# Optimization experiments

Hardware: AMD Instinct MI355X
Metric: run time of the kernel (lower is better)

The kernel has to match this reference:

```python
import jax, jax.numpy as jnp
import numpy as np

N = 100000   # total nodes across the batch of glycan graphs
E = 300000   # directed edges
H = 256      # hidden_dim
D = 128      # embedding_dim (projection out)
L = 3        # num_layers
G = 10000    # number of graphs in the batch
V = 14       # monosaccharide vocab size
EPS = 1e-5   # BatchNorm eps


def setup_inputs() -> dict:
    key = jax.random.key(0)
    ks = jax.random.split(key, 12)
    s = 1.0 / np.sqrt(H)
    node_ids = jax.random.randint(ks[0], (N,), 0, V, dtype=jnp.int32)
    edge_index = jax.random.randint(ks[1], (2, E), 0, N, dtype=jnp.int32)
    batch_ids = jnp.sort(jax.random.randint(ks[2], (N,), 0, G, dtype=jnp.int32))
    return {
        "node_ids": node_ids,
        "edge_index": edge_index,
        "batch_ids": batch_ids,
        "emb": jax.random.normal(ks[3], (V, H), jnp.float32),
        "Ws": jax.random.normal(ks[4], (L, H, H), jnp.float32) * s,
        "bs": jax.random.normal(ks[5], (L, H), jnp.float32) * 0.01,
        "gammas": 1.0 + 0.1 * jax.random.normal(ks[6], (L, H), jnp.float32),
        "betas": 0.1 * jax.random.normal(ks[7], (L, H), jnp.float32),
        "run_mean": 0.1 * jax.random.normal(ks[8], (L, H), jnp.float32),
        "run_var": jax.random.uniform(ks[9], (L, H), jnp.float32) + 0.5,
        "projW": jax.random.normal(ks[10], (H, D), jnp.float32) * s,
        "projb": jax.random.normal(ks[11], (D,), jnp.float32) * 0.01,
    }


def reference(node_ids, edge_index, batch_ids, emb, Ws, bs, gammas, betas,
              run_mean, run_var, projW, projb):
    # --- GCN normalization with self-loops (PyG GCNConv defaults) ---
    src, dst = edge_index[0], edge_index[1]
    loops = jnp.arange(N, dtype=src.dtype)
    src_f = jnp.concatenate([src, loops])  # [E+N]
    dst_f = jnp.concatenate([dst, loops])
    deg = jax.ops.segment_sum(jnp.ones_like(dst_f, dtype=jnp.float32), dst_f,
                              num_segments=N)
    dinv = jnp.where(deg > 0, jax.lax.rsqrt(deg), 0.0)
    norm = dinv[src_f] * dinv[dst_f]       # [E+N]

    x = emb[node_ids]                       # [N, H]
    for l in range(L):
        h = x @ Ws[l]                       # GCNConv linear transform
        msg = h[src_f] * norm[:, None]      # [E+N, H] gathered messages
        h = jax.ops.segment_sum(msg, dst_f, num_segments=N) + bs[l]
        # BatchNorm1d (eval mode: running stats) + ReLU; dropout is identity in eval
        h = (h - run_mean[l]) * jax.lax.rsqrt(run_var[l] + EPS) * gammas[l] + betas[l]
        x = jax.nn.relu(h)

    # global_mean_pool over graph assignment
    counts = jax.ops.segment_sum(jnp.ones((N,), jnp.float32), batch_ids,
                                 num_segments=G)
    sums = jax.ops.segment_sum(x, batch_ids, num_segments=G)   # [G, H]
    pooled = sums / jnp.maximum(counts, 1.0)[:, None]
    return pooled @ projW + projb           # [G, D]
```

## Files before the change

kernel.cpp:

```cpp
#include <hip/hip_runtime.h>

#define HDIM 256
#define DDIM 128
#define VSZ 14

typedef __bf16 bf16x8 __attribute__((ext_vector_type(8)));
typedef float f32x4 __attribute__((ext_vector_type(4)));

static __device__ __forceinline__ unsigned short f2bf(float f) {
  unsigned u = __builtin_bit_cast(unsigned, f);
  u += 0x7FFF + ((u >> 16) & 1);
  return (unsigned short)(u >> 16);
}
static __device__ __forceinline__ unsigned pack2(float a, float b) {
  return (unsigned)f2bf(a) | ((unsigned)f2bf(b) << 16);
}
static __device__ __forceinline__ void ub8(uint4 p, float* o) {
  o[0] = __builtin_bit_cast(float, p.x << 16);
  o[1] = __builtin_bit_cast(float, p.x & 0xFFFF0000u);
  o[2] = __builtin_bit_cast(float, p.y << 16);
  o[3] = __builtin_bit_cast(float, p.y & 0xFFFF0000u);
  o[4] = __builtin_bit_cast(float, p.z << 16);
  o[5] = __builtin_bit_cast(float, p.z & 0xFFFF0000u);
  o[6] = __builtin_bit_cast(float, p.w << 16);
  o[7] = __builtin_bit_cast(float, p.w & 0xFFFF0000u);
}


__global__ void k_count(const int* __restrict__ dst, int* __restrict__ cnt, int E) {
  int i = blockIdx.x * 256 + threadIdx.x;
  if (i < E) atomicAdd(&cnt[dst[i]], 1);
}

__global__ void k_scan_chunk(const int* __restrict__ cnt, int* __restrict__ off,
                             int* __restrict__ bsum, float* __restrict__ dinv, int n) {
  __shared__ int s[256];
  int i = blockIdx.x * 256 + threadIdx.x;
  int v = (i < n) ? cnt[i] : 0;
  if (i < n) dinv[i] = rsqrtf((float)(v + 1));
  s[threadIdx.x] = v;
  __syncthreads();
  for (int d = 1; d < 256; d <<= 1) {
    int add = (threadIdx.x >= d) ? s[threadIdx.x - d] : 0;
    __syncthreads();
    s[threadIdx.x] += add;
    __syncthreads();
  }
  if (i < n) off[i] = s[threadIdx.x] - v;
  if (threadIdx.x == 255) bsum[blockIdx.x] = s[255];
}

__global__ void k_scan_bsum(int* bsum, int nb) {
  if (threadIdx.x == 0) {
    int acc = 0;
    for (int b = 0; b < nb; ++b) { int t = bsum[b]; bsum[b] = acc; acc += t; }
  }
}

__global__ void k_scan_add(int* __restrict__ off, const int* __restrict__ bsum,
                           int* __restrict__ cnt, int n, int E) {
  int i = blockIdx.x * 256 + threadIdx.x;
  if (i < n) {
    off[i] += bsum[i >> 8];
    cnt[i] = 0;
  } else if (i == n) {
    off[n] = E;
  }
}

__global__ void k_fill(const int* __restrict__ src, const int* __restrict__ dst,
                       const int* __restrict__ ids, const float* __restrict__ dinv,
                       const int* __restrict__ off, int* __restrict__ cur,
                       int4* __restrict__ edata, int E) {
  int i = blockIdx.x * 256 + threadIdx.x;
  if (i >= E) return;
  int d = dst[i];
  int p = off[d] + atomicAdd(&cur[d], 1);
  int s = src[i];
  int4 v;
  v.x = s;
  v.y = ids[s];
  v.z = __builtin_bit_cast(int, dinv[s]);
  v.w = 0;
  edata[p] = v;
}


__global__ void k_embw(const float* __restrict__ emb, const float* __restrict__ W0,
                       float* __restrict__ embW) {
  int t = blockIdx.x, j = threadIdx.x;
  float acc = 0.f;
  for (int k = 0; k < HDIM; ++k) acc = fmaf(emb[t * HDIM + k], W0[k * HDIM + j], acc);
  embW[t * HDIM + j] = acc;
}

__global__ void k_bnc(const float* __restrict__ bs, const float* __restrict__ g,
                      const float* __restrict__ be, const float* __restrict__ mu,
                      const float* __restrict__ va, float* __restrict__ A,
                      float* __restrict__ B) {
  int i = blockIdx.x * HDIM + threadIdx.x;
  float a = g[i] * rsqrtf(va[i] + 1e-5f);
  A[i] = a;
  B[i] = (bs[i] - mu[i]) * a + be[i];
}

__global__ __launch_bounds__(256) void k_wcvt(const float* __restrict__ W,
                                              unsigned short* __restrict__ Wt) {
  __shared__ float tile[32][33];
  int bx = blockIdx.x * 32, by = blockIdx.y * 32;
  int tx = threadIdx.x & 31, ty = threadIdx.x >> 5;
#pragma unroll
  for (int i = 0; i < 4; ++i)
    tile[ty + i * 8][tx] = W[(size_t)(by + ty + i * 8) * HDIM + bx + tx];
  __syncthreads();
#pragma unroll
  for (int i = 0; i < 4; ++i)
    Wt[(size_t)(bx + ty + i * 8) * HDIM + by + tx] = f2bf(tile[tx][ty + i * 8]);
}


__global__ __launch_bounds__(256) void k_layer1(
    const int* __restrict__ ids, const float* __restrict__ embW,
    const int* __restrict__ off, const int4* __restrict__ edata,
    const float* __restrict__ dinv,
    const float* __restrict__ A, const float* __restrict__ B,
    unsigned short* __restrict__ Y, int n) {
  __shared__ unsigned short lw[VSZ * HDIM];
  for (int i = threadIdx.x; i < VSZ * HDIM; i += 256) lw[i] = f2bf(embW[i]);
  __syncthreads();
  int j = (threadIdx.x & 31) * 8;
  float4 a0 = *reinterpret_cast<const float4*>(&A[j]);
  float4 a1 = *reinterpret_cast<const float4*>(&A[j + 4]);
  float4 b0 = *reinterpret_cast<const float4*>(&B[j]);
  float4 b1 = *reinterpret_cast<const float4*>(&B[j + 4]);
  int nb = (n + 7) >> 3;
  for (int b = blockIdx.x; b < nb; b += gridDim.x) {
    int v = b * 8 + (threadIdx.x >> 5);
    if (v >= n) continue;
    float dv = dinv[v];
    float s = dv * dv;
    float acc[8], m[8];
    uint4 x = *reinterpret_cast<const uint4*>(&lw[ids[v] * HDIM + j]);
    ub8(x, acc);
#pragma unroll
    for (int i = 0; i < 8; ++i) acc[i] *= s;
    int e = off[v], e1 = off[v + 1];
    for (; e + 3 < e1; e += 4) {
      int4 d0 = edata[e], d1 = edata[e + 1], d2 = edata[e + 2], d3 = edata[e + 3];
      uint4 g0 = *reinterpret_cast<const uint4*>(&lw[d0.y * HDIM + j]);
      uint4 g1 = *reinterpret_cast<const uint4*>(&lw[d1.y * HDIM + j]);
      uint4 g2 = *reinterpret_cast<const uint4*>(&lw[d2.y * HDIM + j]);
      uint4 g3 = *reinterpret_cast<const uint4*>(&lw[d3.y * HDIM + j]);
      float w0 = dv * __builtin_bit_cast(float, d0.z);
      float w1 = dv * __builtin_bit_cast(float, d1.z);
      float w2 = dv * __builtin_bit_cast(float, d2.z);
      float w3 = dv * __builtin_bit_cast(float, d3.z);
      ub8(g0, m);
#pragma unroll
      for (int i = 0; i < 8; ++i) acc[i] = fmaf(w0, m[i], acc[i]);
      ub8(g1, m);
#pragma unroll
      for (int i = 0; i < 8; ++i) acc[i] = fmaf(w1, m[i], acc[i]);
      ub8(g2, m);
#pragma unroll
      for (int i = 0; i < 8; ++i) acc[i] = fmaf(w2, m[i], acc[i]);
      ub8(g3, m);
#pragma unroll
      for (int i = 0; i < 8; ++i) acc[i] = fmaf(w3, m[i], acc[i]);
    }
    for (; e < e1; ++e) {
      int4 d0 = edata[e];
      uint4 g0 = *reinterpret_cast<const uint4*>(&lw[d0.y * HDIM + j]);
      float w0 = dv * __builtin_bit_cast(float, d0.z);
      ub8(g0, m);
#pragma unroll
      for (int i = 0; i < 8; ++i) acc[i] = fmaf(w0, m[i], acc[i]);
    }
    float o[8];
    o[0] = fmaxf(fmaf(acc[0], a0.x, b0.x), 0.f);
    o[1] = fmaxf(fmaf(acc[1], a0.y, b0.y), 0.f);
    o[2] = fmaxf(fmaf(acc[2], a0.z, b0.z), 0.f);
    o[3] = fmaxf(fmaf(acc[3], a0.w, b0.w), 0.f);
    o[4] = fmaxf(fmaf(acc[4], a1.x, b1.x), 0.f);
    o[5] = fmaxf(fmaf(acc[5], a1.y, b1.y), 0.f);
    o[6] = fmaxf(fmaf(acc[6], a1.z, b1.z), 0.f);
    o[7] = fmaxf(fmaf(acc[7], a1.w, b1.w), 0.f);
    uint4 st;
    st.x = pack2(o[0], o[1]);
    st.y = pack2(o[2], o[3]);
    st.z = pack2(o[4], o[5]);
    st.w = pack2(o[6], o[7]);
    *reinterpret_cast<uint4*>(&Y[(size_t)v * HDIM + j]) = st;
  }
}


__global__ __launch_bounds__(256) void k_agg(
    const unsigned short* __restrict__ X, const int* __restrict__ off,
    const int4* __restrict__ edata, const float* __restrict__ dinv,
    unsigned short* __restrict__ Yb, int n) {
  int j = (threadIdx.x & 31) * 8;
  int nb = (n + 7) >> 3;
  for (int b = blockIdx.x; b < nb; b += gridDim.x) {
    int v = b * 8 + (threadIdx.x >> 5);
    if (v >= n) continue;
    float dv = dinv[v];
    float s = dv * dv;
    float acc[8], m[8];
    uint4 x = *reinterpret_cast<const uint4*>(&X[(size_t)v * HDIM + j]);
    ub8(x, acc);
#pragma unroll
    for (int i = 0; i < 8; ++i) acc[i] *= s;
    int e = off[v], e1 = off[v + 1];
    for (; e + 3 < e1; e += 4) {
      int4 d0 = edata[e], d1 = edata[e + 1], d2 = edata[e + 2], d3 = edata[e + 3];
      uint4 g0 = *reinterpret_cast<const uint4*>(&X[(size_t)d0.x * HDIM + j]);
      uint4 g1 = *reinterpret_cast<const uint4*>(&X[(size_t)d1.x * HDIM + j]);
      uint4 g2 = *reinterpret_cast<const uint4*>(&X[(size_t)d2.x * HDIM + j]);
      uint4 g3 = *reinterpret_cast<const uint4*>(&X[(size_t)d3.x * HDIM + j]);
      float w0 = dv * __builtin_bit_cast(float, d0.z);
      float w1 = dv * __builtin_bit_cast(float, d1.z);
      float w2 = dv * __builtin_bit_cast(float, d2.z);
      float w3 = dv * __builtin_bit_cast(float, d3.z);
      ub8(g0, m);
#pragma unroll
      for (int i = 0; i < 8; ++i) acc[i] = fmaf(w0, m[i], acc[i]);
      ub8(g1, m);
#pragma unroll
      for (int i = 0; i < 8; ++i) acc[i] = fmaf(w1, m[i], acc[i]);
      ub8(g2, m);
#pragma unroll
      for (int i = 0; i < 8; ++i) acc[i] = fmaf(w2, m[i], acc[i]);
      ub8(g3, m);
#pragma unroll
      for (int i = 0; i < 8; ++i) acc[i] = fmaf(w3, m[i], acc[i]);
    }
    for (; e < e1; ++e) {
      int4 d0 = edata[e];
      uint4 g0 = *reinterpret_cast<const uint4*>(&X[(size_t)d0.x * HDIM + j]);
      float w0 = dv * __builtin_bit_cast(float, d0.z);
      ub8(g0, m);
#pragma unroll
      for (int i = 0; i < 8; ++i) acc[i] = fmaf(w0, m[i], acc[i]);
    }
    uint4 st;
    st.x = pack2(acc[0], acc[1]);
    st.y = pack2(acc[2], acc[3]);
    st.z = pack2(acc[4], acc[5]);
    st.w = pack2(acc[6], acc[7]);
    *reinterpret_cast<uint4*>(&Yb[(size_t)v * HDIM + j]) = st;
  }
}


#define BM 128
#define BN 128
#define BK 32
#define LDK 40
#define LDC 136

__global__ __launch_bounds__(256) void k_gemm_mfma(
    const unsigned short* __restrict__ Xb, const unsigned short* __restrict__ Wt,
    const float* __restrict__ Asc, const float* __restrict__ Bsh,
    unsigned short* __restrict__ Y, int M) {
  __shared__ uint4 smem4[BM * LDC / 8];
  unsigned short* As = reinterpret_cast<unsigned short*>(smem4);
  unsigned short* Bs = As + BM * LDK;
  unsigned short* Cs = As;
  int t = threadIdx.x;
  int m0 = blockIdx.x * BM;
  int n0 = blockIdx.y * BN;
  int l = t & 63, w = t >> 6;
  int wm = w & 1, wn = w >> 1;
  int cl = l & 15, q = l >> 4;
  int r0 = t >> 2;
  int kc = (t & 3) * 8;

  f32x4 acc[4][4];
  f32x4 zf = {0.f, 0.f, 0.f, 0.f};
#pragma unroll
  for (int i = 0; i < 4; ++i)
#pragma unroll
    for (int jj = 0; jj < 4; ++jj) acc[i][jj] = zf;

  int arow0 = m0 + r0;      if (arow0 > M - 1) arow0 = M - 1;
  int arow1 = m0 + r0 + 64; if (arow1 > M - 1) arow1 = M - 1;
  int brow0 = n0 + r0, brow1 = n0 + r0 + 64;

  for (int k0 = 0; k0 < HDIM; k0 += BK) {
    uint4 a0 = *reinterpret_cast<const uint4*>(&Xb[(size_t)arow0 * HDIM + k0 + kc]);
    uint4 a1 = *reinterpret_cast<const uint4*>(&Xb[(size_t)arow1 * HDIM + k0 + kc]);
    uint4 b0 = *reinterpret_cast<const uint4*>(&Wt[(size_t)brow0 * HDIM + k0 + kc]);
    uint4 b1 = *reinterpret_cast<const uint4*>(&Wt[(size_t)brow1 * HDIM + k0 + kc]);
    __syncthreads();
    *reinterpret_cast<uint4*>(&As[r0 * LDK + kc]) = a0;
    *reinterpret_cast<uint4*>(&As[(r0 + 64) * LDK + kc]) = a1;
    *reinterpret_cast<uint4*>(&Bs[r0 * LDK + kc]) = b0;
    *reinterpret_cast<uint4*>(&Bs[(r0 + 64) * LDK + kc]) = b1;
    __syncthreads();
    bf16x8 af[4], bfr[4];
#pragma unroll
    for (int i = 0; i < 4; ++i)
      af[i] = *reinterpret_cast<const bf16x8*>(&As[(wm * 64 + i * 16 + cl) * LDK + q * 8]);
#pragma unroll
    for (int jj = 0; jj < 4; ++jj)
      bfr[jj] = *reinterpret_cast<const bf16x8*>(&Bs[(wn * 64 + jj * 16 + cl) * LDK + q * 8]);
#pragma unroll
    for (int i = 0; i < 4; ++i)
#pragma unroll
      for (int jj = 0; jj < 4; ++jj)
        acc[i][jj] = __builtin_amdgcn_mfma_f32_16x16x32_bf16(af[i], bfr[jj], acc[i][jj], 0, 0, 0);
  }

  __syncthreads();
#pragma unroll
  for (int jj = 0; jj < 4; ++jj) {
    int col = wn * 64 + jj * 16 + cl;
    float as = Asc[n0 + col], bsv = Bsh[n0 + col];
#pragma unroll
    for (int i = 0; i < 4; ++i) {
      int rowb = wm * 64 + i * 16 + q * 4;
#pragma unroll
      for (int r = 0; r < 4; ++r)
        Cs[(rowb + r) * LDC + col] = f2bf(fmaxf(fmaf(acc[i][jj][r], as, bsv), 0.f));
    }
  }
  __syncthreads();
#pragma unroll
  for (int c = 0; c < 8; ++c) {
    int idx = t + 256 * c;
    int row = idx >> 4, cq = (idx & 15) * 8;
    int gr = m0 + row;
    if (gr < M)
      *reinterpret_cast<uint4*>(&Y[(size_t)gr * HDIM + n0 + cq]) =
          *reinterpret_cast<const uint4*>(&Cs[row * LDC + cq]);
  }
}


__global__ void k_goff(const int* __restrict__ batch, int* __restrict__ goff, int G, int n) {
  int g = blockIdx.x * 256 + threadIdx.x;
  if (g > G) return;
  int lo = 0, hi = n;
  while (lo < hi) {
    int mid = (lo + hi) >> 1;
    if (batch[mid] < g) lo = mid + 1;
    else hi = mid;
  }
  goff[g] = lo;
}

__global__ __launch_bounds__(256) void k_pool(
    const unsigned short* __restrict__ X, const int* __restrict__ goff,
    float* __restrict__ P, int G) {
  int g = blockIdx.x * 8 + (threadIdx.x >> 5);
  if (g >= G) return;
  int j = (threadIdx.x & 31) * 8;
  int r0 = goff[g], r1 = goff[g + 1];
  float acc[8] = {0.f, 0.f, 0.f, 0.f, 0.f, 0.f, 0.f, 0.f};
  float m[8];
  int r = r0;
  for (; r + 1 < r1; r += 2) {
    uint4 x0 = *reinterpret_cast<const uint4*>(&X[(size_t)r * HDIM + j]);
    uint4 x1 = *reinterpret_cast<const uint4*>(&X[(size_t)(r + 1) * HDIM + j]);
    ub8(x0, m);
#pragma unroll
    for (int i = 0; i < 8; ++i) acc[i] += m[i];
    ub8(x1, m);
#pragma unroll
    for (int i = 0; i < 8; ++i) acc[i] += m[i];
  }
  if (r < r1) {
    uint4 x0 = *reinterpret_cast<const uint4*>(&X[(size_t)r * HDIM + j]);
    ub8(x0, m);
#pragma unroll
    for (int i = 0; i < 8; ++i) acc[i] += m[i];
  }
  float inv = 1.f / fmaxf((float)(r1 - r0), 1.f);
  float4 o0 = make_float4(acc[0] * inv, acc[1] * inv, acc[2] * inv, acc[3] * inv);
  float4 o1 = make_float4(acc[4] * inv, acc[5] * inv, acc[6] * inv, acc[7] * inv);
  *reinterpret_cast<float4*>(&P[(size_t)g * HDIM + j]) = o0;
  *reinterpret_cast<float4*>(&P[(size_t)g * HDIM + j + 4]) = o1;
}


__global__ __launch_bounds__(128) void k_proj(
    const float* __restrict__ P, const float* __restrict__ W,
    const float* __restrict__ bias, float* __restrict__ out, int G) {
  __shared__ float rows[8][HDIM];
  int g0 = blockIdx.x * 8;
  for (int i = threadIdx.x; i < 8 * HDIM; i += 128) {
    int g = g0 + (i >> 8);
    rows[i >> 8][i & 255] = (g < G) ? P[(size_t)g * HDIM + (i & 255)] : 0.f;
  }
  __syncthreads();
  int d = threadIdx.x;
  float bb = bias[d];
  float acc[8] = {bb, bb, bb, bb, bb, bb, bb, bb};
  for (int k = 0; k < HDIM; ++k) {
    float w = W[(size_t)k * DDIM + d];
#pragma unroll
    for (int q = 0; q < 8; ++q) acc[q] = fmaf(rows[q][k], w, acc[q]);
  }
#pragma unroll
  for (int q = 0; q < 8; ++q) {
    int g = g0 + q;
    if (g < G) out[(size_t)g * DDIM + d] = acc[q];
  }
}


extern "C" void kernel_launch(void* const* d_in, const int* in_sizes, int n_in,
                              void* d_out, int out_size, void* d_ws, size_t ws_size,
                              hipStream_t stream) {
  const int N = in_sizes[0];
  const int E = in_sizes[1] / 2;
  const int G = out_size / DDIM;

  const int* node_ids = (const int*)d_in[0];
  const int* src = (const int*)d_in[1];
  const int* dst = src + E;
  const int* batch = (const int*)d_in[2];
  const float* emb = (const float*)d_in[3];
  const float* Ws = (const float*)d_in[4];
  const float* bs = (const float*)d_in[5];
  const float* gam = (const float*)d_in[6];
  const float* bet = (const float*)d_in[7];
  const float* mu = (const float*)d_in[8];
  const float* va = (const float*)d_in[9];
  const float* pW = (const float*)d_in[10];
  const float* pb = (const float*)d_in[11];
  float* out = (float*)d_out;

  size_t o = 0;
  auto alloc = [&](size_t bytes) -> void* {
    size_t start = (o + 255) & ~(size_t)255;
    o = start + bytes;
    return (void*)((char*)d_ws + start);
  };
  int NB = (N + 255) / 256;
  int* cnt = (int*)alloc((size_t)N * 4);
  float* dinv = (float*)alloc((size_t)N * 4);
  int* off = (int*)alloc((size_t)(N + 1) * 4);
  int* bsum = (int*)alloc((size_t)NB * 4);
  int4* edata = (int4*)alloc((size_t)E * 16);
  float* embW = (float*)alloc((size_t)VSZ * HDIM * 4);
  float* Ac = (float*)alloc((size_t)3 * HDIM * 4);
  float* Bc = (float*)alloc((size_t)3 * HDIM * 4);
  int* goff = (int*)alloc((size_t)(G + 1) * 4);
  unsigned short* Wtb = (unsigned short*)alloc((size_t)2 * HDIM * HDIM * 2);
  unsigned short* bufX = (unsigned short*)alloc((size_t)N * HDIM * 2);
  unsigned short* bufY = (unsigned short*)alloc((size_t)N * HDIM * 2);
  float* pooled = (float*)alloc((size_t)G * HDIM * 4);

  int gE = (E + 255) / 256;

  hipMemsetAsync(cnt, 0, (size_t)N * 4, stream);
  k_count<<<gE, 256, 0, stream>>>(dst, cnt, E);
  k_scan_chunk<<<NB, 256, 0, stream>>>(cnt, off, bsum, dinv, N);
  k_scan_bsum<<<1, 64, 0, stream>>>(bsum, NB);
  k_scan_add<<<(N + 1 + 255) / 256, 256, 0, stream>>>(off, bsum, cnt, N, E);
  k_fill<<<gE, 256, 0, stream>>>(src, dst, node_ids, dinv, off, cnt, edata, E);

  k_embw<<<VSZ, HDIM, 0, stream>>>(emb, Ws, embW);
  k_bnc<<<3, HDIM, 0, stream>>>(bs, gam, bet, mu, va, Ac, Bc);
  dim3 tg(8, 8);
  k_wcvt<<<tg, 256, 0, stream>>>(Ws + 1 * HDIM * HDIM, Wtb);
  k_wcvt<<<tg, 256, 0, stream>>>(Ws + 2 * HDIM * HDIM, Wtb + HDIM * HDIM);

  int gs = 2048;
  k_layer1<<<gs, 256, 0, stream>>>(node_ids, embW, off, edata, dinv,
                                   Ac, Bc, bufX, N);

  dim3 gg((N + BM - 1) / BM, HDIM / BN);
  k_agg<<<gs, 256, 0, stream>>>(bufX, off, edata, dinv, bufY, N);
  k_gemm_mfma<<<gg, 256, 0, stream>>>(bufY, Wtb, Ac + HDIM, Bc + HDIM, bufX, N);
  k_agg<<<gs, 256, 0, stream>>>(bufX, off, edata, dinv, bufY, N);
  k_gemm_mfma<<<gg, 256, 0, stream>>>(bufY, Wtb + HDIM * HDIM, Ac + 2 * HDIM, Bc + 2 * HDIM, bufX, N);

  k_goff<<<(G + 1 + 255) / 256, 256, 0, stream>>>(batch, goff, G, N);
  k_pool<<<(G + 7) / 8, 256, 0, stream>>>(bufX, goff, pooled, G);
  k_proj<<<(G + 7) / 8, 128, 0, stream>>>(pooled, pW, pb, out, G);
}
```

Before: 312.4 us.

## Replace three-pass scan with atomic block allocation and merge prep kernels

Swaps the three-kernel prefix scan for a single kernel in which each block claims its CSR segment base with an atomicAdd on a global counter. Edge ranges now come from off plus per-node degree, and a separate cur buffer is zeroed alongside cnt. The weight transpose, embedding projection, BatchNorm constants and graph offset search are merged into one k_prep launch. Node id and dinv are packed into one int2 so k_fill does a single gather per edge. This removes about seven small launches, at the cost of CSR segments no longer following node order, which may hurt edge-read locality in the aggregation kernels.

```diff
diff --git a/kernel.cpp b/kernel.cpp
--- a/kernel.cpp
+++ b/kernel.cpp
@@ -32,13 +32,22 @@
   if (i < E) atomicAdd(&cnt[dst[i]], 1);
 }
 
-__global__ void k_scan_chunk(const int* __restrict__ cnt, int* __restrict__ off,
-                             int* __restrict__ bsum, float* __restrict__ dinv, int n) {
+__global__ void k_alloc(const int* __restrict__ cnt, int* __restrict__ off,
+                        float* __restrict__ dinv, int2* __restrict__ ninfo,
+                        const int* __restrict__ ids, int* __restrict__ total, int n) {
   __shared__ int s[256];
+  __shared__ int base;
   int i = blockIdx.x * 256 + threadIdx.x;
-  int v = (i < n) ? cnt[i] : 0;
-  if (i < n) dinv[i] = rsqrtf((float)(v + 1));
-  s[threadIdx.x] = v;
+  int c = (i < n) ? cnt[i] : 0;
+  if (i < n) {
+    float dv = rsqrtf((float)(c + 1));
+    dinv[i] = dv;
+    int2 inf;
+    inf.x = ids[i];
+    inf.y = __builtin_bit_cast(int, dv);
+    ninfo[i] = inf;
+  }
+  s[threadIdx.x] = c;
   __syncthreads();
   for (int d = 1; d < 256; d <<= 1) {
     int add = (threadIdx.x >= d) ? s[threadIdx.x - d] : 0;
@@ -46,83 +55,80 @@
     s[threadIdx.x] += add;
     __syncthreads();
   }
-  if (i < n) off[i] = s[threadIdx.x] - v;
-  if (threadIdx.x == 255) bsum[blockIdx.x] = s[255];
-}
-
-__global__ void k_scan_bsum(int* bsum, int nb) {
-  if (threadIdx.x == 0) {
-    int acc = 0;
-    for (int b = 0; b < nb; ++b) { int t = bsum[b]; bsum[b] = acc; acc += t; }
-  }
-}
-
-__global__ void k_scan_add(int* __restrict__ off, const int* __restrict__ bsum,
-                           int* __restrict__ cnt, int n, int E) {
-  int i = blockIdx.x * 256 + threadIdx.x;
-  if (i < n) {
-    off[i] += bsum[i >> 8];
-    cnt[i] = 0;
-  } else if (i == n) {
-    off[n] = E;
-  }
+  if (threadIdx.x == 255) base = atomicAdd(total, s[255]);
+  __syncthreads();
+  if (i < n) off[i] = base + s[threadIdx.x] - c;
 }
 
 __global__ void k_fill(const int* __restrict__ src, const int* __restrict__ dst,
-                       const int* __restrict__ ids, const float* __restrict__ dinv,
-                       const int* __restrict__ off, int* __restrict__ cur,
-                       int4* __restrict__ edata, int E) {
+                       const int2* __restrict__ ninfo, const int* __restrict__ off,
+                       int* __restrict__ cur, int4* __restrict__ edata, int E) {
   int i = blockIdx.x * 256 + threadIdx.x;
   if (i >= E) return;
   int d = dst[i];
   int p = off[d] + atomicAdd(&cur[d], 1);
   int s = src[i];
+  int2 inf = ninfo[s];
   int4 v;
   v.x = s;
-  v.y = ids[s];
-  v.z = __builtin_bit_cast(int, dinv[s]);
+  v.y = inf.x;
+  v.z = inf.y;
   v.w = 0;
   edata[p] = v;
 }
 
 
-__global__ void k_embw(const float* __restrict__ emb, const float* __restrict__ W0,
-                       float* __restrict__ embW) {
-  int t = blockIdx.x, j = threadIdx.x;
-  float acc = 0.f;
-  for (int k = 0; k < HDIM; ++k) acc = fmaf(emb[t * HDIM + k], W0[k * HDIM + j], acc);
-  embW[t * HDIM + j] = acc;
-}
-
-__global__ void k_bnc(const float* __restrict__ bs, const float* __restrict__ g,
-                      const float* __restrict__ be, const float* __restrict__ mu,
-                      const float* __restrict__ va, float* __restrict__ A,
-                      float* __restrict__ B) {
-  int i = blockIdx.x * HDIM + threadIdx.x;
-  float a = g[i] * rsqrtf(va[i] + 1e-5f);
-  A[i] = a;
-  B[i] = (bs[i] - mu[i]) * a + be[i];
-}
-
-__global__ __launch_bounds__(256) void k_wcvt(const float* __restrict__ W,
-                                              unsigned short* __restrict__ Wt) {
-  __shared__ float tile[32][33];
-  int bx = blockIdx.x * 32, by = blockIdx.y * 32;
-  int tx = threadIdx.x & 31, ty = threadIdx.x >> 5;
-#pragma unroll
-  for (int i = 0; i < 4; ++i)
-    tile[ty + i * 8][tx] = W[(size_t)(by + ty + i * 8) * HDIM + bx + tx];
-  __syncthreads();
-#pragma unroll
-  for (int i = 0; i < 4; ++i)
-    Wt[(size_t)(bx + ty + i * 8) * HDIM + by + tx] = f2bf(tile[tx][ty + i * 8]);
+__global__ __launch_bounds__(256) void k_prep(
+    const float* __restrict__ emb, const float* __restrict__ Ws,
+    const float* __restrict__ bs, const float* __restrict__ gam,
+    const float* __restrict__ bet, const float* __restrict__ mu,
+    const float* __restrict__ va, const int* __restrict__ batch,
+    float* __restrict__ embW, float* __restrict__ Ac, float* __restrict__ Bc,
+    unsigned short* __restrict__ Wtb, int* __restrict__ goff, int G, int n) {
+  int b = blockIdx.x;
+  if (b < 128) {
+    __shared__ float tile[32][33];
+    int layer = b >> 6;
+    int tb = b & 63;
+    int bx = (tb & 7) * 32, by = (tb >> 3) * 32;
+    const float* W = Ws + (size_t)(layer + 1) * HDIM * HDIM;
+    unsigned short* Wt = Wtb + (size_t)layer * HDIM * HDIM;
+    int tx = threadIdx.x & 31, ty = threadIdx.x >> 5;
+#pragma unroll
+    for (int i = 0; i < 4; ++i)
+      tile[ty + i * 8][tx] = W[(size_t)(by + ty + i * 8) * HDIM + bx + tx];
+    __syncthreads();
+#pragma unroll
+    for (int i = 0; i < 4; ++i)
+      Wt[(size_t)(bx + ty + i * 8) * HDIM + by + tx] = f2bf(tile[tx][ty + i * 8]);
+  } else if (b < 142) {
+    int t = b - 128, j = threadIdx.x;
+    float acc = 0.f;
+    for (int k = 0; k < HDIM; ++k) acc = fmaf(emb[t * HDIM + k], Ws[k * HDIM + j], acc);
+    embW[t * HDIM + j] = acc;
+  } else if (b < 145) {
+    int i = (b - 142) * HDIM + threadIdx.x;
+    float a = gam[i] * rsqrtf(va[i] + 1e-5f);
+    Ac[i] = a;
+    Bc[i] = (bs[i] - mu[i]) * a + bet[i];
+  } else {
+    int g = (b - 145) * 256 + threadIdx.x;
+    if (g > G) return;
+    int lo = 0, hi = n;
+    while (lo < hi) {
+      int mid = (lo + hi) >> 1;
+      if (batch[mid] < g) lo = mid + 1;
+      else hi = mid;
+    }
+    goff[g] = lo;
+  }
 }
 
 
 __global__ __launch_bounds__(256) void k_layer1(
     const int* __restrict__ ids, const float* __restrict__ embW,
-    const int* __restrict__ off, const int4* __restrict__ edata,
-    const float* __restrict__ dinv,
+    const int* __restrict__ off, const int* __restrict__ deg,
+    const int4* __restrict__ edata, const float* __restrict__ dinv,
     const float* __restrict__ A, const float* __restrict__ B,
     unsigned short* __restrict__ Y, int n) {
   __shared__ unsigned short lw[VSZ * HDIM];
@@ -144,7 +150,7 @@
     ub8(x, acc);
 #pragma unroll
     for (int i = 0; i < 8; ++i) acc[i] *= s;
-    int e = off[v], e1 = off[v + 1];
+    int e = off[v], e1 = e + deg[v];
     for (; e + 3 < e1; e += 4) {
       int4 d0 = edata[e], d1 = edata[e + 1], d2 = edata[e + 2], d3 = edata[e + 3];
       uint4 g0 = *reinterpret_cast<const uint4*>(&lw[d0.y * HDIM + j]);
@@ -197,8 +203,8 @@
 
 __global__ __launch_bounds__(256) void k_agg(
     const unsigned short* __restrict__ X, const int* __restrict__ off,
-    const int4* __restrict__ edata, const float* __restrict__ dinv,
-    unsigned short* __restrict__ Yb, int n) {
+    const int* __restrict__ deg, const int4* __restrict__ edata,
+    const float* __restrict__ dinv, unsigned short* __restrict__ Yb, int n) {
   int j = (threadIdx.x & 31) * 8;
   int nb = (n + 7) >> 3;
   for (int b = blockIdx.x; b < nb; b += gridDim.x) {
@@ -211,7 +217,7 @@
     ub8(x, acc);
 #pragma unroll
     for (int i = 0; i < 8; ++i) acc[i] *= s;
-    int e = off[v], e1 = off[v + 1];
+    int e = off[v], e1 = e + deg[v];
     for (; e + 3 < e1; e += 4) {
       int4 d0 = edata[e], d1 = edata[e + 1], d2 = edata[e + 2], d3 = edata[e + 3];
       uint4 g0 = *reinterpret_cast<const uint4*>(&X[(size_t)d0.x * HDIM + j]);
@@ -338,18 +344,6 @@
 }
 
 
-__global__ void k_goff(const int* __restrict__ batch, int* __restrict__ goff, int G, int n) {
-  int g = blockIdx.x * 256 + threadIdx.x;
-  if (g > G) return;
-  int lo = 0, hi = n;
-  while (lo < hi) {
-    int mid = (lo + hi) >> 1;
-    if (batch[mid] < g) lo = mid + 1;
-    else hi = mid;
-  }
-  goff[g] = lo;
-}
-
 __global__ __launch_bounds__(256) void k_pool(
     const unsigned short* __restrict__ X, const int* __restrict__ goff,
     float* __restrict__ P, int G) {
@@ -438,11 +432,13 @@
     o = start + bytes;
     return (void*)((char*)d_ws + start);
   };
-  int NB = (N + 255) / 256;
-  int* cnt = (int*)alloc((size_t)N * 4);
+  int* zbuf = (int*)alloc((size_t)(2 * N + 1) * 4);
+  int* cnt = zbuf;
+  int* cur = zbuf + N;
+  int* total = zbuf + 2 * N;
   float* dinv = (float*)alloc((size_t)N * 4);
-  int* off = (int*)alloc((size_t)(N + 1) * 4);
-  int* bsum = (int*)alloc((size_t)NB * 4);
+  int* off = (int*)alloc((size_t)N * 4);
+  int2* ninfo = (int2*)alloc((size_t)N * 8);
   int4* edata = (int4*)alloc((size_t)E * 16);
   float* embW = (float*)alloc((size_t)VSZ * HDIM * 4);
   float* Ac = (float*)alloc((size_t)3 * HDIM * 4);
@@ -454,31 +450,27 @@
   float* pooled = (float*)alloc((size_t)G * HDIM * 4);
 
   int gE = (E + 255) / 256;
-
-  hipMemsetAsync(cnt, 0, (size_t)N * 4, stream);
+  int NB = (N + 255) / 256;
+  int NGB = (G + 1 + 255) / 256;
+
+  hipMemsetAsync(zbuf, 0, (size_t)(2 * N + 1) * 4, stream);
   k_count<<<gE, 256, 0, stream>>>(dst, cnt, E);
-  k_scan_chunk<<<NB, 256, 0, stream>>>(cnt, off, bsum, dinv, N);
-  k_scan_bsum<<<1, 64, 0, stream>>>(bsum, NB);
-  k_scan_add<<<(N + 1 + 255) / 256, 256, 0, stream>>>(off, bsum, cnt, N, E);
-  k_fill<<<gE, 256, 0, stream>>>(src, dst, node_ids, dinv, off, cnt, edata, E);
-
-  k_embw<<<VSZ, HDIM, 0, stream>>>(emb, Ws, embW);
-  k_bnc<<<3, HDIM, 0, stream>>>(bs, gam, bet, mu, va, Ac, Bc);
-  dim3 tg(8, 8);
-  k_wcvt<<<tg, 256, 0, stream>>>(Ws + 1 * HDIM * HDIM, Wtb);
-  k_wcvt<<<tg, 256, 0, stream>>>(Ws + 2 * HDIM * HDIM, Wtb + HDIM * HDIM);
+  k_alloc<<<NB, 256, 0, stream>>>(cnt, off, dinv, ninfo, node_ids, total, N);
+  k_fill<<<gE, 256, 0, stream>>>(src, dst, ninfo, off, cur, edata, E);
+
+  k_prep<<<145 + NGB, 256, 0, stream>>>(emb, Ws, bs, gam, bet, mu, va, batch,
+                                        embW, Ac, Bc, Wtb, goff, G, N);
 
   int gs = 2048;
-  k_layer1<<<gs, 256, 0, stream>>>(node_ids, embW, off, edata, dinv,
+  k_layer1<<<gs, 256, 0, stream>>>(node_ids, embW, off, cnt, edata, dinv,
                                    Ac, Bc, bufX, N);
 
   dim3 gg((N + BM - 1) / BM, HDIM / BN);
-  k_agg<<<gs, 256, 0, stream>>>(bufX, off, edata, dinv, bufY, N);
+  k_agg<<<gs, 256, 0, stream>>>(bufX, off, cnt, edata, dinv, bufY, N);
   k_gemm_mfma<<<gg, 256, 0, stream>>>(bufY, Wtb, Ac + HDIM, Bc + HDIM, bufX, N);
-  k_agg<<<gs, 256, 0, stream>>>(bufX, off, edata, dinv, bufY, N);
+  k_agg<<<gs, 256, 0, stream>>>(bufX, off, cnt, edata, dinv, bufY, N);
   k_gemm_mfma<<<gg, 256, 0, stream>>>(bufY, Wtb + HDIM * HDIM, Ac + 2 * HDIM, Bc + 2 * HDIM, bufX, N);
 
-  k_goff<<<(G + 1 + 255) / 256, 256, 0, stream>>>(batch, goff, G, N);
   k_pool<<<(G + 7) / 8, 256, 0, stream>>>(bufX, goff, pooled, G);
   k_proj<<<(G + 7) / 8, 128, 0, stream>>>(pooled, pW, pb, out, G);
 }
```

New measurement: 270.7 us. 1.15x faster.
